# Optimization experiments

Measured on AMD Instinct MI355X. Metric: run time of the kernel, lower is better.

Reference implementation:

```python
import jax, jax.numpy as jnp
import numpy as np

NEG_BIG = -9e15
ALPHA = 0.2  # LeakyReLU negative slope


def setup_inputs() -> dict:
    key = jax.random.key(0)
    k1, k2, k3, k4 = jax.random.split(key, 4)
    B, N, IN, OUT = 8, 2048, 128, 64
    x = jax.random.normal(k1, (B, N, IN), dtype=jnp.float32)
    adj = jax.random.randint(k2, (B, N, N), 0, 2, dtype=jnp.int32)
    # xavier_uniform with gain=1.414
    lim_W = 1.414 * np.sqrt(6.0 / (IN + OUT))
    W = jax.random.uniform(k3, (IN, OUT), jnp.float32, -lim_W, lim_W)
    lim_a = 1.414 * np.sqrt(6.0 / (2 * OUT + 1))
    a = jax.random.uniform(k4, (2 * OUT, 1), jnp.float32, -lim_a, lim_a)
    return {"x": x, "adj": adj, "W": W, "a": a}


def reference(x, adj, W, a):
    # h: [B, N, out_dim]
    h = jnp.matmul(x, W)
    out_dim = W.shape[1]
    a1 = a[:out_dim, 0]   # applied to h_i (row / destination)
    a2 = a[out_dim:, 0]   # applied to h_j (col / source)
    # e_ij = leakyrelu(h_i . a1 + h_j . a2)  -- avoids the O(B*N*N*2d) concat
    si = jnp.einsum('bnd,d->bn', h, a1)  # [B, N]
    sj = jnp.einsum('bnd,d->bn', h, a2)  # [B, N]
    e = si[:, :, None] + sj[:, None, :]  # [B, N, N]
    e = jnp.where(e > 0, e, ALPHA * e)   # LeakyReLU
    e = jnp.where(adj > 0, e, NEG_BIG)
    attention = jax.nn.softmax(e, axis=-1)  # [B, N, N]
    # dropout p=0.0 (eval mode): identity
    h_prime = jnp.matmul(attention, h)       # [B, N, out_dim]
    return h_prime, attention
```

## Files before the change

### kernel.cpp

```cpp
#include <hip/hip_runtime.h>

#define BB 8
#define NN 2048
#define IND 128
#define OUTD 64
#define ALPHA 0.2f

typedef __attribute__((ext_vector_type(8))) short bf16x8;
typedef __attribute__((ext_vector_type(4))) float f32x4;
typedef __attribute__((ext_vector_type(4))) int i32x4;
typedef unsigned int u32;

__global__ __launch_bounds__(256) void k1_hproj(const float* __restrict__ x,
                                                const float* __restrict__ W,
                                                const float* __restrict__ a,
                                                short* __restrict__ hT_hi,
                                                short* __restrict__ hT_lo,
                                                float* __restrict__ si,
                                                float* __restrict__ sj) {
    __shared__ float Wl[IND * OUTD];
    __shared__ float xl[16][IND];
    __shared__ float tile[16][OUTD + 1];
    int t = threadIdx.x, lane = t & 63, wave = t >> 6;

    const float4* W4 = (const float4*)W;
    float4* Wl4 = (float4*)Wl;
    #pragma unroll
    for (int q = 0; q < 8; ++q) Wl4[t + q * 256] = W4[t + q * 256];

    int row0 = blockIdx.x * 16;
    const float4* x4 = (const float4*)(x + (size_t)row0 * IND);
    float4* xl4 = (float4*)&xl[0][0];
    xl4[t] = x4[t];
    xl4[t + 256] = x4[t + 256];
    __syncthreads();

    float a1v = a[lane];
    float a2v = a[OUTD + lane];

    float acc[4] = {0.f, 0.f, 0.f, 0.f};
    int rbase = wave * 4;
    for (int k = 0; k < IND; k += 4) {
        float4 xv0 = *(const float4*)&xl[rbase + 0][k];
        float4 xv1 = *(const float4*)&xl[rbase + 1][k];
        float4 xv2 = *(const float4*)&xl[rbase + 2][k];
        float4 xv3 = *(const float4*)&xl[rbase + 3][k];
        #pragma unroll
        for (int q = 0; q < 4; ++q) {
            float w = Wl[(k + q) * OUTD + lane];
            acc[0] = fmaf(((const float*)&xv0)[q], w, acc[0]);
            acc[1] = fmaf(((const float*)&xv1)[q], w, acc[1]);
            acc[2] = fmaf(((const float*)&xv2)[q], w, acc[2]);
            acc[3] = fmaf(((const float*)&xv3)[q], w, acc[3]);
        }
    }
    #pragma unroll
    for (int rr = 0; rr < 4; ++rr) {
        size_t grow = (size_t)row0 + rbase + rr;
        tile[rbase + rr][lane] = acc[rr];
        float v1 = acc[rr] * a1v;
        float v2 = acc[rr] * a2v;
        #pragma unroll
        for (int o = 32; o; o >>= 1) {
            v1 += __shfl_xor(v1, o);
            v2 += __shfl_xor(v2, o);
        }
        if (lane == 0) { si[grow] = v1; sj[grow] = v2; }
    }
    __syncthreads();

    int d = t >> 2, kq = (t & 3) * 4;
    int b = row0 >> 11;
    int krow = (row0 & (NN - 1)) + kq;
    float v0 = tile[kq + 0][d], v1 = tile[kq + 1][d];
    float v2 = tile[kq + 2][d], v3 = tile[kq + 3][d];
    u32 b0 = __float_as_uint(v0), b1 = __float_as_uint(v1);
    u32 b2 = __float_as_uint(v2), b3 = __float_as_uint(v3);
    u32 h0 = b0 & 0xffff0000u, h1 = b1 & 0xffff0000u;
    u32 h2 = b2 & 0xffff0000u, h3 = b3 & 0xffff0000u;
    float l0 = v0 - __uint_as_float(h0), l1 = v1 - __uint_as_float(h1);
    float l2 = v2 - __uint_as_float(h2), l3 = v3 - __uint_as_float(h3);
    uint2 hi2, lo2;
    hi2.x = (b0 >> 16) | h1;
    hi2.y = (b2 >> 16) | h3;
    lo2.x = (__float_as_uint(l0) >> 16) | (__float_as_uint(l1) & 0xffff0000u);
    lo2.y = (__float_as_uint(l2) >> 16) | (__float_as_uint(l3) & 0xffff0000u);
    size_t off = ((size_t)b * OUTD + d) * NN + krow;
    *(uint2*)(hT_hi + off) = hi2;
    *(uint2*)(hT_lo + off) = lo2;
}

__global__ __launch_bounds__(256) void k23(const int* __restrict__ adj,
                                           const float* __restrict__ si,
                                           const float* __restrict__ sj,
                                           float* __restrict__ invS,
                                           unsigned char* __restrict__ mask,
                                           float* __restrict__ attn) {
    int t = threadIdx.x, lane = t & 63, w = t >> 6;
    int row0 = (blockIdx.x * 4 + w) * 4;
    int b = row0 >> 11;
    const f32x4* sjb4 = (const f32x4*)(sj + ((size_t)b << 11));

    f32x4 sv[8];
    #pragma unroll
    for (int q = 0; q < 8; ++q) sv[q] = sjb4[q * 64 + lane];

    i32x4 buf[8];
    {
        const i32x4* a0 = (const i32x4*)(adj + (size_t)row0 * NN);
        #pragma unroll
        for (int q = 0; q < 8; ++q) buf[q] = a0[q * 64 + lane];
    }

    #pragma unroll
    for (int r = 0; r < 4; ++r) {
        int row = row0 + r;
        float s_i = si[row];

        u32 nib = 0;
        float sum = 0.f;
        #pragma unroll
        for (int q = 0; q < 8; ++q) {
            i32x4 A = buf[q];
            f32x4 s = sv[q];
            float e, pe;
            e = s_i + s.x; e = e > 0.f ? e : ALPHA * e; pe = __expf(e);
            if (A.x > 0) { nib |= 1u << (q * 4 + 0); sum += pe; }
            e = s_i + s.y; e = e > 0.f ? e : ALPHA * e; pe = __expf(e);
            if (A.y > 0) { nib |= 1u << (q * 4 + 1); sum += pe; }
            e = s_i + s.z; e = e > 0.f ? e : ALPHA * e; pe = __expf(e);
            if (A.z > 0) { nib |= 1u << (q * 4 + 2); sum += pe; }
            e = s_i + s.w; e = e > 0.f ? e : ALPHA * e; pe = __expf(e);
            if (A.w > 0) { nib |= 1u << (q * 4 + 3); sum += pe; }
        }

        if (r < 3) {
            const i32x4* an = (const i32x4*)(adj + (size_t)(row + 1) * NN);
            #pragma unroll
            for (int q = 0; q < 8; ++q) buf[q] = an[q * 64 + lane];
        }

        #pragma unroll
        for (int o = 32; o; o >>= 1) sum += __shfl_xor(sum, o);
        float inv = sum > 0.f ? 1.0f / sum : 0.f;
        if (lane == 0) invS[row] = inv;

        #pragma unroll
        for (int q = 0; q < 8; ++q) {
            u32 n0 = (nib >> (q * 4)) & 0xFu;
            u32 pn = (u32)__shfl_xor((int)n0, 1);
            if (!(lane & 1))
                mask[(size_t)row * 256 + q * 32 + (lane >> 1)] =
                    (unsigned char)(n0 | (pn << 4));
        }

        float* orow = attn + (size_t)row * NN;
        #pragma unroll
        for (int q = 0; q < 8; ++q) {
            f32x4 s = sv[q];
            u32 n = nib >> (q * 4);
            f32x4 pv;
            float e;
            e = s_i + s.x; e = e > 0.f ? e : ALPHA * e;
            pv.x = (n & 1u) ? __expf(e) * inv : 0.f;
            e = s_i + s.y; e = e > 0.f ? e : ALPHA * e;
            pv.y = (n & 2u) ? __expf(e) * inv : 0.f;
            e = s_i + s.z; e = e > 0.f ? e : ALPHA * e;
            pv.z = (n & 4u) ? __expf(e) * inv : 0.f;
            e = s_i + s.w; e = e > 0.f ? e : ALPHA * e;
            pv.w = (n & 8u) ? __expf(e) * inv : 0.f;
            *(f32x4*)(orow + q * 256 + lane * 4) = pv;
        }
    }
}

__global__ __launch_bounds__(256) void k4_pv(const unsigned char* __restrict__ mask,
                                             const float* __restrict__ si,
                                             const float* __restrict__ sj,
                                             const float* __restrict__ invS,
                                             const short* __restrict__ hT_hi,
                                             const short* __restrict__ hT_lo,
                                             float* __restrict__ hp) {
    __shared__ f32x4 red[4][4][64];

    int t = threadIdx.x, lane = t & 63, w = t >> 6;
    int bk = blockIdx.x;
    int b = bk >> 7;
    int i0 = (bk & 127) * 16;
    size_t rowbase = (size_t)b * NN + i0;
    const float* sjb = sj + (size_t)b * NN;

    int m = lane & 15, g = lane >> 4;
    float si_m = si[rowbase + m];
    float inv_m = invS[rowbase + m];
    const unsigned char* mrow = mask + (rowbase + m) * 256;
    const short* bh0 = hT_hi + ((size_t)b * OUTD + m) * NN;
    const short* bl0 = hT_lo + ((size_t)b * OUTD + m) * NN;

    f32x4 acc[4];
    #pragma unroll
    for (int tt = 0; tt < 4; ++tt) acc[tt] = (f32x4){0.f, 0.f, 0.f, 0.f};

    #pragma unroll 2
    for (int step = 0; step < 16; ++step) {
        int kk = w * 512 + step * 32;
        int c0 = kk + g * 8;
        unsigned mb = mrow[(kk >> 3) + g];
        f32x4 s0 = *(const f32x4*)(sjb + c0);
        f32x4 s1 = *(const f32x4*)(sjb + c0 + 4);
        float sv[8] = {s0.x, s0.y, s0.z, s0.w, s1.x, s1.y, s1.z, s1.w};
        float p[8];
        #pragma unroll
        for (int q = 0; q < 8; ++q) {
            float e = si_m + sv[q];
            e = e > 0.f ? e : ALPHA * e;
            float pe = __expf(e) * inv_m;
            p[q] = ((mb >> q) & 1u) ? pe : 0.f;
        }

        union { bf16x8 v; u32 u[4]; } ph, pl;
        #pragma unroll
        for (int q = 0; q < 4; ++q) {
            u32 c0u = __float_as_uint(p[2 * q]), c1u = __float_as_uint(p[2 * q + 1]);
            u32 t0 = c0u & 0xffff0000u, t1 = c1u & 0xffff0000u;
            float d0 = p[2 * q] - __uint_as_float(t0);
            float d1 = p[2 * q + 1] - __uint_as_float(t1);
            ph.u[q] = (c0u >> 16) | t1;
            pl.u[q] = (__float_as_uint(d0) >> 16) | (__float_as_uint(d1) & 0xffff0000u);
        }

        #pragma unroll
        for (int tt = 0; tt < 4; ++tt) {
            bf16x8 bh = *(const bf16x8*)(bh0 + (size_t)tt * 16 * NN + c0);
            bf16x8 bl = *(const bf16x8*)(bl0 + (size_t)tt * 16 * NN + c0);
            acc[tt] = __builtin_amdgcn_mfma_f32_16x16x32_bf16(ph.v, bh, acc[tt], 0, 0, 0);
            acc[tt] = __builtin_amdgcn_mfma_f32_16x16x32_bf16(ph.v, bl, acc[tt], 0, 0, 0);
            acc[tt] = __builtin_amdgcn_mfma_f32_16x16x32_bf16(pl.v, bh, acc[tt], 0, 0, 0);
        }
    }

    #pragma unroll
    for (int tt = 0; tt < 4; ++tt) red[w][tt][lane] = acc[tt];
    __syncthreads();

    for (int idx = t; idx < 16 * OUTD; idx += 256) {
        int row = idx >> 6, n = idx & 63;
        int ln = (row >> 2) * 16 + (n & 15);
        int reg = row & 3;
        float v = ((const float*)&red[0][n >> 4][ln])[reg]
                + ((const float*)&red[1][n >> 4][ln])[reg]
                + ((const float*)&red[2][n >> 4][ln])[reg]
                + ((const float*)&red[3][n >> 4][ln])[reg];
        hp[(rowbase + row) * OUTD + n] = v;
    }
}

extern "C" void kernel_launch(void* const* d_in, const int* in_sizes, int n_in,
                              void* d_out, int out_size, void* d_ws, size_t ws_size,
                              hipStream_t stream) {
    const float* x   = (const float*)d_in[0];
    const int*   adj = (const int*)d_in[1];
    const float* W   = (const float*)d_in[2];
    const float* a   = (const float*)d_in[3];

    float* out  = (float*)d_out;
    float* hp   = out;
    float* attn = out + (size_t)BB * NN * OUTD;

    char* ws = (char*)d_ws;
    short* hT_hi = (short*)ws;
    short* hT_lo = hT_hi + (size_t)BB * OUTD * NN;
    float* si    = (float*)(hT_lo + (size_t)BB * OUTD * NN);
    float* sj    = si + (size_t)BB * NN;
    float* invS  = sj + (size_t)BB * NN;
    unsigned char* mask = (unsigned char*)(invS + (size_t)BB * NN);

    k1_hproj<<<BB * NN / 16, 256, 0, stream>>>(x, W, a, hT_hi, hT_lo, si, sj);
    k23<<<BB * NN / 16, 256, 0, stream>>>(adj, si, sj, invS, mask, attn);
    k4_pv<<<BB * NN / 16, 256, 0, stream>>>(mask, si, sj, invS, hT_hi, hT_lo, hp);
}
```

Measured before the change: 154.7 us.

## Cache exp values, store mask as per-lane words, halve rows per wave

The softmax kernel now keeps the 32 exponentials per lane in registers instead of recomputing them for the attention write. The mask is stored as one 32-bit nibble word per lane, which removes the shuffles and byte stores, and the PV kernel decodes 8 mask bits from a uint2 load. Each wave now handles 2 rows instead of 4 and the grid is doubled, giving more parallelism at the cost of more sj reloads per row and higher register pressure.

```diff
diff --git a/kernel.cpp b/kernel.cpp
--- a/kernel.cpp
+++ b/kernel.cpp
@@ -94,10 +94,10 @@
                                            const float* __restrict__ si,
                                            const float* __restrict__ sj,
                                            float* __restrict__ invS,
-                                           unsigned char* __restrict__ mask,
+                                           u32* __restrict__ mask32,
                                            float* __restrict__ attn) {
     int t = threadIdx.x, lane = t & 63, w = t >> 6;
-    int row0 = (blockIdx.x * 4 + w) * 4;
+    int row0 = (blockIdx.x * 4 + w) * 2;
     int b = row0 >> 11;
     const f32x4* sjb4 = (const f32x4*)(sj + ((size_t)b << 11));
 
@@ -113,28 +113,29 @@
     }
 
     #pragma unroll
-    for (int r = 0; r < 4; ++r) {
+    for (int r = 0; r < 2; ++r) {
         int row = row0 + r;
         float s_i = si[row];
 
         u32 nib = 0;
         float sum = 0.f;
+        float pe[32];
         #pragma unroll
         for (int q = 0; q < 8; ++q) {
             i32x4 A = buf[q];
             f32x4 s = sv[q];
-            float e, pe;
-            e = s_i + s.x; e = e > 0.f ? e : ALPHA * e; pe = __expf(e);
-            if (A.x > 0) { nib |= 1u << (q * 4 + 0); sum += pe; }
-            e = s_i + s.y; e = e > 0.f ? e : ALPHA * e; pe = __expf(e);
-            if (A.y > 0) { nib |= 1u << (q * 4 + 1); sum += pe; }
-            e = s_i + s.z; e = e > 0.f ? e : ALPHA * e; pe = __expf(e);
-            if (A.z > 0) { nib |= 1u << (q * 4 + 2); sum += pe; }
-            e = s_i + s.w; e = e > 0.f ? e : ALPHA * e; pe = __expf(e);
-            if (A.w > 0) { nib |= 1u << (q * 4 + 3); sum += pe; }
-        }
-
-        if (r < 3) {
+            float e;
+            e = s_i + s.x; e = e > 0.f ? e : ALPHA * e; pe[q * 4 + 0] = __expf(e);
+            if (A.x > 0) { nib |= 1u << (q * 4 + 0); sum += pe[q * 4 + 0]; }
+            e = s_i + s.y; e = e > 0.f ? e : ALPHA * e; pe[q * 4 + 1] = __expf(e);
+            if (A.y > 0) { nib |= 1u << (q * 4 + 1); sum += pe[q * 4 + 1]; }
+            e = s_i + s.z; e = e > 0.f ? e : ALPHA * e; pe[q * 4 + 2] = __expf(e);
+            if (A.z > 0) { nib |= 1u << (q * 4 + 2); sum += pe[q * 4 + 2]; }
+            e = s_i + s.w; e = e > 0.f ? e : ALPHA * e; pe[q * 4 + 3] = __expf(e);
+            if (A.w > 0) { nib |= 1u << (q * 4 + 3); sum += pe[q * 4 + 3]; }
+        }
+
+        if (r < 1) {
             const i32x4* an = (const i32x4*)(adj + (size_t)(row + 1) * NN);
             #pragma unroll
             for (int q = 0; q < 8; ++q) buf[q] = an[q * 64 + lane];
@@ -144,37 +145,23 @@
         for (int o = 32; o; o >>= 1) sum += __shfl_xor(sum, o);
         float inv = sum > 0.f ? 1.0f / sum : 0.f;
         if (lane == 0) invS[row] = inv;
-
+        mask32[(size_t)row * 64 + lane] = nib;
+
+        float* orow = attn + (size_t)row * NN;
         #pragma unroll
         for (int q = 0; q < 8; ++q) {
-            u32 n0 = (nib >> (q * 4)) & 0xFu;
-            u32 pn = (u32)__shfl_xor((int)n0, 1);
-            if (!(lane & 1))
-                mask[(size_t)row * 256 + q * 32 + (lane >> 1)] =
-                    (unsigned char)(n0 | (pn << 4));
-        }
-
-        float* orow = attn + (size_t)row * NN;
-        #pragma unroll
-        for (int q = 0; q < 8; ++q) {
-            f32x4 s = sv[q];
             u32 n = nib >> (q * 4);
             f32x4 pv;
-            float e;
-            e = s_i + s.x; e = e > 0.f ? e : ALPHA * e;
-            pv.x = (n & 1u) ? __expf(e) * inv : 0.f;
-            e = s_i + s.y; e = e > 0.f ? e : ALPHA * e;
-            pv.y = (n & 2u) ? __expf(e) * inv : 0.f;
-            e = s_i + s.z; e = e > 0.f ? e : ALPHA * e;
-            pv.z = (n & 4u) ? __expf(e) * inv : 0.f;
-            e = s_i + s.w; e = e > 0.f ? e : ALPHA * e;
-            pv.w = (n & 8u) ? __expf(e) * inv : 0.f;
+            pv.x = (n & 1u) ? pe[q * 4 + 0] * inv : 0.f;
+            pv.y = (n & 2u) ? pe[q * 4 + 1] * inv : 0.f;
+            pv.z = (n & 4u) ? pe[q * 4 + 2] * inv : 0.f;
+            pv.w = (n & 8u) ? pe[q * 4 + 3] * inv : 0.f;
             *(f32x4*)(orow + q * 256 + lane * 4) = pv;
         }
     }
 }
 
-__global__ __launch_bounds__(256) void k4_pv(const unsigned char* __restrict__ mask,
+__global__ __launch_bounds__(256) void k4_pv(const u32* __restrict__ mask32,
                                              const float* __restrict__ si,
                                              const float* __restrict__ sj,
                                              const float* __restrict__ invS,
@@ -193,7 +180,7 @@
     int m = lane & 15, g = lane >> 4;
     float si_m = si[rowbase + m];
     float inv_m = invS[rowbase + m];
-    const unsigned char* mrow = mask + (rowbase + m) * 256;
+    const u32* mrow = mask32 + (rowbase + m) * 64;
     const short* bh0 = hT_hi + ((size_t)b * OUTD + m) * NN;
     const short* bl0 = hT_lo + ((size_t)b * OUTD + m) * NN;
 
@@ -205,7 +192,11 @@
     for (int step = 0; step < 16; ++step) {
         int kk = w * 512 + step * 32;
         int c0 = kk + g * 8;
-        unsigned mb = mrow[(kk >> 3) + g];
+        int q8 = c0 >> 8;
+        int widx = (c0 & 255) >> 2;
+        uint2 wp = *(const uint2*)&mrow[widx];
+        unsigned mb = ((wp.x >> (q8 * 4)) & 0xFu) | (((wp.y >> (q8 * 4)) & 0xFu) << 4);
+
         f32x4 s0 = *(const f32x4*)(sjb + c0);
         f32x4 s1 = *(const f32x4*)(sjb + c0 + 4);
         float sv[8] = {s0.x, s0.y, s0.z, s0.w, s1.x, s1.y, s1.z, s1.w};
@@ -273,9 +264,9 @@
     float* si    = (float*)(hT_lo + (size_t)BB * OUTD * NN);
     float* sj    = si + (size_t)BB * NN;
     float* invS  = sj + (size_t)BB * NN;
-    unsigned char* mask = (unsigned char*)(invS + (size_t)BB * NN);
+    u32*   mask32 = (u32*)(invS + (size_t)BB * NN);
 
     k1_hproj<<<BB * NN / 16, 256, 0, stream>>>(x, W, a, hT_hi, hT_lo, si, sj);
-    k23<<<BB * NN / 16, 256, 0, stream>>>(adj, si, sj, invS, mask, attn);
-    k4_pv<<<BB * NN / 16, 256, 0, stream>>>(mask, si, sj, invS, hT_hi, hT_lo, hp);
-}
+    k23<<<BB * NN / 8, 256, 0, stream>>>(adj, si, sj, invS, mask32, attn);
+    k4_pv<<<BB * NN / 16, 256, 0, stream>>>(mask32, si, sj, invS, hT_hi, hT_lo, hp);
+}
```

Result: no change. 156.0 us (+0.8%).
